# Optimization experiments

Hardware: AMD Instinct MI355X
Metric: run time of the kernel (lower is better)

## Reference

```python
import jax, jax.numpy as jnp
import numpy as np

B, T, IDIM, HDIM, K, LMAX, NLAYERS = 64, 1024, 120, 320, 72, 96, 3
LAMB = 0.1
NEG = -1e30


def lse3(a, b, c):
    m = jnp.maximum(jnp.maximum(a, b), c)
    return m + jnp.log(jnp.exp(a - m) + jnp.exp(b - m) + jnp.exp(c - m))


def _lstm_dir(x, Wih, Whh, bb):
    # x: [B,T,D] -> h: [B,T,H]; PyTorch gate order i,f,g,o
    gx = jnp.einsum('btd,gd->tbg', x, Wih) + bb  # [T,B,4H]
    def step(carry, g):
        h, c = carry
        g = g + h @ Whh.T
        i, f, gg, o = jnp.split(g, 4, axis=-1)
        c = jax.nn.sigmoid(f) * c + jax.nn.sigmoid(i) * jnp.tanh(gg)
        h = jax.nn.sigmoid(o) * jnp.tanh(c)
        return (h, c), h
    h0 = jnp.zeros((x.shape[0], HDIM), x.dtype)
    _, hs = jax.lax.scan(step, (h0, h0), gx)
    return hs.transpose(1, 0, 2)


def _rev(x, lengths):
    # reverse each sequence within its valid length (packed-sequence semantics)
    t = jnp.arange(x.shape[1])
    idx = jnp.where(t[None, :] < lengths[:, None], lengths[:, None] - 1 - t[None, :], t[None, :])
    return jnp.take_along_axis(x, idx[:, :, None], axis=1)


def _blstm_layer(x, Wih_f, Whh_f, b_f, Wih_b, Whh_b, b_b, lengths):
    hf = _lstm_dir(x, Wih_f, Whh_f, b_f)
    hb = _rev(_lstm_dir(_rev(x, lengths), Wih_b, Whh_b, b_b), lengths)
    return jnp.concatenate([hf, hb], axis=2)


def _ctc_forward(logp, labels, in_lens, lab_lens):
    # standard CTC alpha recursion (blank=0), log-space, vectorized over batch
    Bn, Tn, _ = logp.shape
    S = 2 * LMAX + 1
    ext = jnp.zeros((Bn, S), jnp.int32).at[:, 1::2].set(labels)  # blank-interleaved labels
    em = jnp.take_along_axis(logp, jnp.broadcast_to(ext[:, None, :], (Bn, Tn, S)), axis=2)
    em = em.transpose(1, 0, 2)  # [T,B,S]
    s_idx = jnp.arange(S)
    prev_lab = jnp.concatenate([jnp.full((Bn, 2), -1, jnp.int32), ext[:, :-2]], axis=1)
    can_skip = ((s_idx[None, :] % 2) == 1) & (ext != prev_lab)
    valid_s = s_idx[None, :] < (2 * lab_lens[:, None] + 1)
    alpha0 = jnp.full((Bn, S), NEG, logp.dtype)
    alpha0 = alpha0.at[:, 0].set(em[0][:, 0]).at[:, 1].set(em[0][:, 1])
    alpha0 = jnp.where(valid_s, alpha0, NEG)
    def step(alpha, inp):
        em_t, t = inp
        a2 = jnp.concatenate([jnp.full((Bn, 1), NEG, alpha.dtype), alpha[:, :-1]], axis=1)
        a3 = jnp.concatenate([jnp.full((Bn, 2), NEG, alpha.dtype), alpha[:, :-2]], axis=1)
        a3 = jnp.where(can_skip, a3, NEG)
        new = lse3(alpha, a2, a3) + em_t
        new = jnp.where(valid_s, new, NEG)
        new = jnp.where((t < in_lens)[:, None], new, alpha)  # freeze past utterance end
        return new, None
    alpha, _ = jax.lax.scan(step, alpha0, (em[1:], jnp.arange(1, Tn)))
    last = 2 * lab_lens
    aL = jnp.take_along_axis(alpha, last[:, None], axis=1)[:, 0]
    aLm1 = jnp.take_along_axis(alpha, (last - 1)[:, None], axis=1)[:, 0]
    return jnp.logaddexp(aL, aLm1)  # log p(labels | x)


def setup_inputs():
    key = jax.random.key(0)
    ks = jax.random.split(key, 12)
    H4 = 4 * HDIM
    s = 0.05
    return dict(
        logits=jax.random.normal(ks[0], (B, T, IDIM), jnp.float32),
        labels_padded=jax.random.randint(ks[1], (B, LMAX), 1, K).astype(jnp.int32),
        input_lengths=jax.random.randint(ks[2], (B,), T // 2, T + 1).astype(jnp.int32),
        label_lengths=jax.random.randint(ks[3], (B,), LMAX // 2, LMAX + 1).astype(jnp.int32),
        Wih0=jax.random.normal(ks[4], (2, H4, IDIM), jnp.float32) * s,
        Whh0=jax.random.normal(ks[5], (2, H4, HDIM), jnp.float32) * s,
        b0=jnp.zeros((2, H4), jnp.float32),
        Wih=jax.random.normal(ks[6], (NLAYERS - 1, 2, H4, 2 * HDIM), jnp.float32) * s,
        Whh=jax.random.normal(ks[7], (NLAYERS - 1, 2, H4, HDIM), jnp.float32) * s,
        b=jnp.zeros((NLAYERS - 1, 2, H4), jnp.float32),
        W_lin=jax.random.normal(ks[8], (K, 2 * HDIM), jnp.float32) * s,
        b_lin=jnp.zeros((K,), jnp.float32),
    )


def reference(logits, labels_padded, input_lengths, label_lengths, Wih0, Whh0, b0, Wih, Whh, b, W_lin, b_lin):
    # sort by input length descending (mirrors torch.sort + index_select)
    order = jnp.argsort(-input_lengths)
    logits = logits[order]
    labels_padded = labels_padded[order]
    input_lengths = input_lengths[order]
    label_lengths = label_lengths[order]
    # 3-layer BLSTM encoder
    x = _blstm_layer(logits, Wih0[0], Whh0[0], b0[0], Wih0[1], Whh0[1], b0[1], input_lengths)
    for l in range(NLAYERS - 1):
        x = _blstm_layer(x, Wih[l, 0], Whh[l, 0], b[l, 0], Wih[l, 1], Whh[l, 1], b[l, 1], input_lengths)
    netout = jax.nn.log_softmax(x @ W_lin.T + b_lin, axis=2)  # [B,T,K]
    # CTC-CRF: numerator = CTC alpha log-prob; denominator = free-running partition
    num = _ctc_forward(netout, labels_padded, input_lengths, label_lengths)
    tmask = jnp.arange(netout.shape[1])[None, :] < input_lengths[:, None]
    den = jnp.sum(jnp.where(tmask, jax.nn.logsumexp(netout, axis=2), 0.0), axis=1)
    return jnp.mean(den - (1.0 + LAMB) * num)
```

## Files before the change

kernel.cpp:

```cpp
#include <hip/hip_runtime.h>
#include <cstdint>
#include <cstddef>


typedef _Float16 f16;
typedef _Float16 h2v   __attribute__((ext_vector_type(2)));
typedef _Float16 f16x4v __attribute__((ext_vector_type(4)));
typedef _Float16 f16x8 __attribute__((ext_vector_type(8)));
typedef float    f32x4 __attribute__((ext_vector_type(4)));
typedef uint32_t u32x4 __attribute__((ext_vector_type(4)));

#define NEGF (-1e30f)
#define CT 128

__device__ __forceinline__ float dot2f(h2v a, h2v b, float c) {
#if __has_builtin(__builtin_amdgcn_fdot2)
  return __builtin_amdgcn_fdot2(a, b, c, false);
#else
  return c + (float)a.x * (float)b.x + (float)a.y * (float)b.y;
#endif
}

__device__ __forceinline__ float fast_rcp(float x) {
#if __has_builtin(__builtin_amdgcn_rcpf)
  return __builtin_amdgcn_rcpf(x);
#else
  return 1.f / x;
#endif
}
__device__ __forceinline__ float fsigm(float x) { return fast_rcp(1.f + __expf(-x)); }
__device__ __forceinline__ float ftanh(float x) { return 1.f - 2.f * fast_rcp(1.f + __expf(2.f * x)); }

__device__ __forceinline__ float fexp2(float x) {
#if __has_builtin(__builtin_amdgcn_exp2f)
  return __builtin_amdgcn_exp2f(x);
#else
  return exp2f(x);
#endif
}
__device__ __forceinline__ float flog2(float x) {
#if __has_builtin(__builtin_amdgcn_logf)
  return __builtin_amdgcn_logf(x);
#else
  return log2f(x);
#endif
}

__device__ __forceinline__ void bar_lds() {
  __builtin_amdgcn_sched_barrier(0);
  asm volatile("s_waitcnt lgkmcnt(0)" ::: "memory");
  __builtin_amdgcn_s_barrier();
  __builtin_amdgcn_sched_barrier(0);
}

__device__ __forceinline__ void stage16(f16* lds, const f16* g) {
#if __has_builtin(__builtin_amdgcn_global_load_lds)
  __builtin_amdgcn_global_load_lds(
      (const __attribute__((address_space(1))) uint32_t*)g,
      (__attribute__((address_space(3))) uint32_t*)lds, 16, 0, 0);
#else
  int lane = threadIdx.x & 63;
  *(f16x8*)&lds[lane * 8] = *(const f16x8*)g;
#endif
}


__global__ void conv_logits(const float* __restrict__ src, f16* __restrict__ dst) {
  int idx = blockIdx.x * 256 + threadIdx.x;
  int row = idx >> 7, k = idx & 127;
  dst[idx] = (f16)((k < 120) ? src[(size_t)row * 120 + k] : 0.f);
}

__global__ void conv_wt0(const float* __restrict__ w, f16* __restrict__ dst) {
  int idx = blockIdx.x * 256 + threadIdx.x;
  int n = idx >> 7, k = idx & 127;
  dst[idx] = (f16)((k < 120) ? w[(size_t)n * 120 + k] : 0.f);
}

__global__ void conv_copy(const float* __restrict__ src, f16* __restrict__ dst, int count) {
  int idx = blockIdx.x * 256 + threadIdx.x;
  if (idx < count) dst[idx] = (f16)src[idx];
}

__global__ void conv_wtl(const float* __restrict__ w, f16* __restrict__ dst) {
  int idx = blockIdx.x * 256 + threadIdx.x;
  int n = idx / 640, k = idx % 640;
  dst[idx] = (f16)((n < 72) ? w[(size_t)n * 640 + k] : 0.f);
}

__global__ void conv_whh(const float* __restrict__ whh0, const float* __restrict__ whh,
                         uint32_t* __restrict__ dst) {
  int o = blockIdx.x * 256 + threadIdx.x;
  int tid = o & 511;
  int g  = o >> 9;
  int j  = g % 40;
  int g2 = g / 40;
  int i  = g2 % 5;
  int g3 = g2 / 5;
  int hf = g3 & 1, slot = g3 >> 1;
  int tau = i * 512 + tid;
  int lr = tau >> 2, kq = tau & 3;
  int gate = lr / 160, u = lr - gate * 160;
  int r = gate * 320 + hf * 160 + u;
  int k = kq * 80 + j * 2;
  const float* srcm = (slot < 2) ? (whh0 + ((size_t)slot * 1280 + r) * 320)
                                 : (whh  + ((size_t)(slot - 2) * 1280 + r) * 320);
  f16 lo = (f16)srcm[k], hi = (f16)srcm[k + 1];
  dst[o] = (uint32_t)__builtin_bit_cast(unsigned short, lo) |
           ((uint32_t)__builtin_bit_cast(unsigned short, hi) << 16);
}

__global__ __launch_bounds__(256)
void gemm_chunk(const f16* __restrict__ A, const f16* __restrict__ W,
                f16* __restrict__ gxc, const int* __restrict__ lens,
                int lda, int kTiles, int c0) {
  __shared__ __align__(16) f16 As[128 * 32];
  __shared__ __align__(16) f16 Ws[2][128 * 32];
  const int tid = threadIdx.x;
  const int lane = tid & 63, wid = tid >> 6;
  const int wm = wid >> 1, wn = wid & 1;
  const int dir = blockIdx.y >> 6, b = blockIdx.y & 63;
  const int n0 = blockIdx.x * 256;
  const int r_base = lane >> 2;
  const int chs = ((((lane & 3) + (r_base >> 1)) & 3)) * 8;
  const int len = lens[b];

  f32x4 acc[4][8] = {};

  for (int kt = 0; kt < kTiles; ++kt) {
    const int k0 = kt * 32;
    __syncthreads();
#pragma unroll
    for (int hh = 0; hh < 2; ++hh) {
      const int c = wid * 2 + hh;
      const int j = c * 16 + r_base;
      const int s = c0 * CT + j;
      const int tt = dir ? ((s < len) ? (len - 1 - s) : s) : s;
      stage16(&As[c * 512], A + (size_t)(b * 1024 + tt) * lda + k0 + chs);
    }
#pragma unroll
    for (int hh = 0; hh < 4; ++hh) {
      const int c = wid * 4 + hh;
      const int tile = c >> 3, cc = c & 7;
      stage16(&Ws[tile][cc * 512],
              W + (size_t)(dir * 1280 + n0 + tile * 128 + cc * 16 + r_base) * lda + k0 + chs);
    }
    __syncthreads();

    const int q = lane >> 4;
    const int l15 = lane & 15;
    const int cs = (q - (l15 >> 1)) & 3;
    const int rofs = l15 * 32 + cs * 8;
    f16x8 av[4], wv0[4], wv1[4];
#pragma unroll
    for (int i = 0; i < 4; ++i)
      av[i] = *(const f16x8*)&As[(wm * 4 + i) * 512 + rofs];
#pragma unroll
    for (int i = 0; i < 4; ++i) {
      wv0[i] = *(const f16x8*)&Ws[0][(wn * 4 + i) * 512 + rofs];
      wv1[i] = *(const f16x8*)&Ws[1][(wn * 4 + i) * 512 + rofs];
    }
#pragma unroll
    for (int i = 0; i < 4; ++i)
#pragma unroll
      for (int j = 0; j < 4; ++j) {
        acc[i][j]     = __builtin_amdgcn_mfma_f32_16x16x32_f16(av[i], wv0[j], acc[i][j], 0, 0, 0);
        acc[i][4 + j] = __builtin_amdgcn_mfma_f32_16x16x32_f16(av[i], wv1[j], acc[i][4 + j], 0, 0, 0);
      }
  }

  const int r0 = (lane >> 4) * 4, cn = lane & 15;
  const size_t obase = (size_t)(dir * 64 + b) * CT;
#pragma unroll
  for (int i = 0; i < 4; ++i) {
    const int m = wm * 64 + i * 16 + r0;
#pragma unroll
    for (int j = 0; j < 4; ++j) {
      const int n = n0 + wn * 64 + j * 16 + cn;
#pragma unroll
      for (int r = 0; r < 4; ++r) {
        gxc[(obase + m + r) * 1280 + n]       = (f16)acc[i][j][r];
        gxc[(obase + m + r) * 1280 + n + 128] = (f16)acc[i][4 + j][r];
      }
    }
  }
}

__global__ void __launch_bounds__(512)
__attribute__((amdgpu_waves_per_eu(2, 2)))
lstm_scan_chunk(const volatile uint32_t* wbuf,
                const f16* __restrict__ gxc,
                const float* __restrict__ bias,
                const int* __restrict__ lens,
                f16* xnext,
                uint32_t* xq,
                f16* hsave,
                float* csave,
                int layer, int c0) {
  const int wg = blockIdx.x;
  const int half = wg >> 7;
  const int bd = wg & 127;
  const int b = bd >> 1, dir = bd & 1;
  const int tid = threadIdx.x;

  __shared__ __align__(16) f16 hbuf[320];
  __shared__ float ylds[640];
  __shared__ __align__(16) f16 hstage[64 * 160];

  h2v w[5][40];
  {
    const volatile uint32_t* wb =
        wbuf + (size_t)((layer * 2 + dir) * 2 + half) * 200 * 512;
#pragma unroll
    for (int i = 0; i < 5; ++i)
#pragma unroll
      for (int j = 0; j < 40; ++j) {
        uint32_t v = wb[(i * 40 + j) * 512 + tid];
        w[i][j] = __builtin_bit_cast(h2v, v);
      }
  }
  if (tid < 320) hbuf[tid] = (c0 == 0) ? (f16)0.f : hsave[bd * 320 + tid];

  const int len = lens[b];
  const int kq = tid & 3;
  const int qi = tid >> 2;
  const int gu = half * 160 + tid;
  float c_state = 0.f;
  float bi = 0.f, bff = 0.f, bg = 0.f, bo = 0.f;
  if (tid < 160) {
    if (c0 > 0) c_state = csave[wg * 160 + tid];
    const float* bp = bias + dir * 1280 + gu;
    bi = bp[0]; bff = bp[320]; bg = bp[640]; bo = bp[960];
  }
  __syncthreads();

  const size_t grow0 = (size_t)(dir * 64 + b) * CT;

  float gxi = 0.f, gxf = 0.f, gxg = 0.f, gxo = 0.f;
  if (tid < 160) {
    const f16* gp = gxc + grow0 * 1280 + gu;
    gxi = (float)gp[0]; gxf = (float)gp[320]; gxg = (float)gp[640]; gxo = (float)gp[960];
  }

  for (int tl = 0; tl < CT; ++tl) {
    const int s = c0 * CT + tl;
    const uint32_t tag = (uint32_t)(layer * 1024 + s + 1);

    float nxi = 0.f, nxf = 0.f, nxg = 0.f, nxo = 0.f;
    if (tid < 160 && tl + 1 < CT) {
      const f16* gp = gxc + (grow0 + tl + 1) * 1280 + gu;
      nxi = (float)gp[0]; nxf = (float)gp[320]; nxg = (float)gp[640]; nxo = (float)gp[960];
    }

    float a0 = 0.f, a1 = 0.f, a2 = 0.f, a3 = 0.f, a4 = 0.f;
    {
      const u32x4* h4 = (const u32x4*)hbuf;
#pragma unroll
      for (int jb = 0; jb < 5; ++jb) {
        u32x4 p = h4[kq * 10 + jb * 2];
        u32x4 q = h4[kq * 10 + jb * 2 + 1];
        h2v hr[8];
#pragma unroll
        for (int j = 0; j < 4; ++j) hr[j] = __builtin_bit_cast(h2v, p[j]);
#pragma unroll
        for (int j = 0; j < 4; ++j) hr[4 + j] = __builtin_bit_cast(h2v, q[j]);
#pragma unroll
        for (int j = 0; j < 8; ++j) {
          a0 = dot2f(w[0][jb * 8 + j], hr[j], a0);
          a1 = dot2f(w[1][jb * 8 + j], hr[j], a1);
          a2 = dot2f(w[2][jb * 8 + j], hr[j], a2);
          a3 = dot2f(w[3][jb * 8 + j], hr[j], a3);
          a4 = dot2f(w[4][jb * 8 + j], hr[j], a4);
        }
      }
    }
    {
      float av[5] = {a0, a1, a2, a3, a4};
#pragma unroll
      for (int i = 0; i < 5; ++i) {
        float v = av[i];
        v += __shfl_xor(v, 1, 64);
        v += __shfl_xor(v, 2, 64);
        if (kq == 0) ylds[i * 128 + qi] = v;
      }
    }

    if ((tl & 31) == 0 && tl > 0) {
      const int tw = tl - 32;
#pragma unroll
      for (int it = 0; it < 2; ++it) {
        const int slot = it * 512 + tid;
        if (slot < 640) {
          const int r = (int)(((unsigned)slot * 52429u) >> 20);
          const int j = slot - r * 20;
          const int sp = c0 * CT + tw + r;
          const int ttp = dir ? ((sp < len) ? (len - 1 - sp) : sp) : sp;
          f16x8 v = *(const f16x8*)&hstage[((tw + r) & 63) * 160 + j * 8];
          *(f16x8*)&xnext[(size_t)(b * 1024 + ttp) * 640 + dir * 320 + half * 160 + j * 8] = v;
        }
      }
    }
    bar_lds();

    if (tid < 160) {
      const int u = tid;
      float pi = ylds[u]       + gxi + bi;
      float pf = ylds[160 + u] + gxf + bff;
      float pg = ylds[320 + u] + gxg + bg;
      float po = ylds[480 + u] + gxo + bo;
      float ig = fsigm(pi);
      float fg = fsigm(pf);
      float gg = ftanh(pg);
      float og = fsigm(po);
      c_state = fg * c_state + ig * gg;
      float hv = og * ftanh(c_state);
      const f16 hh = (f16)hv;
      const uint32_t word = (tag << 16) |
                            (uint32_t)__builtin_bit_cast(unsigned short, hh);
      __hip_atomic_store(&xq[((bd * 2 + half) * 2 + (s & 1)) * 160 + u], word,
                         __ATOMIC_RELAXED, __HIP_MEMORY_SCOPE_AGENT);
      hbuf[gu] = hh;
      hstage[(tl & 63) * 160 + u] = hh;
    } else if (tid >= 256 && tid < 416) {
      const int u = tid - 256;
      uint32_t pw;
      int spins = 0;
      do {
        pw = __hip_atomic_load(&xq[((bd * 2 + (1 - half)) * 2 + (s & 1)) * 160 + u],
                               __ATOMIC_RELAXED, __HIP_MEMORY_SCOPE_AGENT);
      } while ((pw >> 16) != tag && ++spins < 200000);
      hbuf[(1 - half) * 160 + u] =
          __builtin_bit_cast(f16, (unsigned short)(pw & 0xffffu));
    }
    bar_lds();

    gxi = nxi; gxf = nxf; gxg = nxg; gxo = nxo;
  }

  {
    const int tw = CT - 32;
#pragma unroll
    for (int it = 0; it < 2; ++it) {
      const int slot = it * 512 + tid;
      if (slot < 640) {
        const int r = (int)(((unsigned)slot * 52429u) >> 20);
        const int j = slot - r * 20;
        const int sp = c0 * CT + tw + r;
        const int ttp = dir ? ((sp < len) ? (len - 1 - sp) : sp) : sp;
        f16x8 v = *(const f16x8*)&hstage[((tw + r) & 63) * 160 + j * 8];
        *(f16x8*)&xnext[(size_t)(b * 1024 + ttp) * 640 + dir * 320 + half * 160 + j * 8] = v;
      }
    }
  }
  if (tid < 160) {
    hsave[bd * 320 + gu] = hbuf[gu];
    csave[wg * 160 + tid] = c_state;
  }
}

__global__ __launch_bounds__(256)
void gemm_proj(const f16* __restrict__ A, const f16* __restrict__ W,
               float* __restrict__ outf, int lda, int kTiles, int ldo) {
  __shared__ __align__(16) f16 As[128 * 32];
  __shared__ __align__(16) f16 Ws[128 * 32];
  const int tid = threadIdx.x;
  const int lane = tid & 63, wid = tid >> 6;
  const int wm = wid >> 1, wn = wid & 1;
  const int m0 = blockIdx.y * 128, n0 = blockIdx.x * 128;
  const int r_base = lane >> 2;
  const int chs = ((((lane & 3) + (r_base >> 1)) & 3)) * 8;

  f32x4 acc[4][4] = {};

  for (int kt = 0; kt < kTiles; ++kt) {
    const int k0 = kt * 32;
    __syncthreads();
#pragma unroll
    for (int hh = 0; hh < 2; ++hh) {
      const int c = wid * 2 + hh;
      stage16(&As[c * 512], A + (size_t)(m0 + c * 16 + r_base) * lda + k0 + chs);
      stage16(&Ws[c * 512], W + (size_t)(n0 + c * 16 + r_base) * lda + k0 + chs);
    }
    __syncthreads();

    const int q = lane >> 4;
    const int l15 = lane & 15;
    const int cs = (q - (l15 >> 1)) & 3;
    const int rofs = l15 * 32 + cs * 8;
    f16x8 av[4], wv[4];
#pragma unroll
    for (int i = 0; i < 4; ++i)
      av[i] = *(const f16x8*)&As[(wm * 4 + i) * 512 + rofs];
#pragma unroll
    for (int i = 0; i < 4; ++i)
      wv[i] = *(const f16x8*)&Ws[(wn * 4 + i) * 512 + rofs];
#pragma unroll
    for (int i = 0; i < 4; ++i)
#pragma unroll
      for (int j = 0; j < 4; ++j)
        acc[i][j] = __builtin_amdgcn_mfma_f32_16x16x32_f16(av[i], wv[j], acc[i][j], 0, 0, 0);
  }

  const int r0 = (lane >> 4) * 4, cn = lane & 15;
#pragma unroll
  for (int i = 0; i < 4; ++i) {
    const int m = m0 + wm * 64 + i * 16 + r0;
#pragma unroll
    for (int j = 0; j < 4; ++j) {
      const int n = n0 + wn * 64 + j * 16 + cn;
#pragma unroll
      for (int r = 0; r < 4; ++r)
        outf[(size_t)(m + r) * ldo + n] = acc[i][j][r];
    }
  }
}

__global__ void lse_kernel(const float* __restrict__ Z, const float* __restrict__ b_lin,
                           float* __restrict__ lseout) {
  int row = blockIdx.x * 4 + (threadIdx.x >> 6);
  int l = threadIdx.x & 63;
  const float* z = Z + (size_t)row * 128;
  float v0 = (l < 72) ? z[l] + b_lin[l] : NEGF;
  float v1 = (l < 8) ? z[l + 64] + b_lin[l + 64] : NEGF;
  float m = fmaxf(v0, v1);
#pragma unroll
  for (int o = 32; o; o >>= 1) m = fmaxf(m, __shfl_xor(m, o, 64));
  float s = ((l < 72) ? __expf(v0 - m) : 0.f) + ((l < 8) ? __expf(v1 - m) : 0.f);
#pragma unroll
  for (int o = 32; o; o >>= 1) s += __shfl_xor(s, o, 64);
  if (l == 0) lseout[row] = m + __logf(s);
}

__global__ void emz_kernel(const float* __restrict__ Z, const float* __restrict__ lse,
                           const float* __restrict__ b_lin,
                           const int* __restrict__ labels,
                           f16* __restrict__ emc) {
  const int b = blockIdx.y;
  const int t0 = blockIdx.x * 4;
  const int tid = threadIdx.x;
  __shared__ int ext[200];
  __shared__ float bls[200];
  if (tid < 200) {
    int e = (tid < 193 && (tid & 1)) ? labels[b * 96 + (tid >> 1)] : 0;
    ext[tid] = e;
    bls[tid] = b_lin[e];
  }
  __syncthreads();
#pragma unroll
  for (int dt = 0; dt < 4; ++dt) {
    const int t = t0 + dt;
    const float lst = lse[b * 1024 + t];
    const float* zr = Z + ((size_t)(b * 1024 + t)) * 128;
    for (int s = tid; s < 200; s += 256)
      emc[((size_t)(b * 1024 + t)) * 200 + s] =
          (f16)((zr[ext[s]] + bls[s] - lst) * 1.4426950408889634f);
  }
}

__global__ void ctc_kernel(const f16* __restrict__ emc,
                           const int* __restrict__ labels, const int* __restrict__ inlen,
                           const int* __restrict__ lablen, float* __restrict__ num) {
  const int b = blockIdx.x;
  const int lane = threadIdx.x;
  __shared__ int ext[200];
  __shared__ float afin[200];

  for (int s = lane; s < 200; s += 64)
    ext[s] = (s < 193 && (s & 1)) ? labels[b * 96 + (s >> 1)] : 0;
  __syncthreads();

  const int L = lablen[b], len = inlen[b];
  const int Send = 2 * L + 1;
  const f16* eb = emc + (size_t)b * 1024 * 200;

  float a[4];
  bool  skp[4], val[4];
#pragma unroll
  for (int j = 0; j < 4; ++j) {
    const int s = lane * 4 + j;
    val[j] = (s < Send) && (s < 193);
    skp[j] = (s < 193) && (s & 1) && (s >= 2) && (ext[s] != ext[s - 2]);
  }
  {
    f16x4v e0 = *(const f16x4v*)&eb[lane * 4];
#pragma unroll
    for (int j = 0; j < 4; ++j) {
      const int s = lane * 4 + j;
      a[j] = (s <= 1 && val[j]) ? (float)e0[j] : NEGF;
    }
  }

  auto step = [&](f16x4v ev) {
    float p3 = __shfl_up(a[3], 1, 64);
    float p2 = __shfl_up(a[2], 1, 64);
    if (lane == 0) { p3 = NEGF; p2 = NEGF; }
    const float x2[4] = {p3, a[0], a[1], a[2]};
    const float x3[4] = {p2, p3, a[0], a[1]};
#pragma unroll
    for (int j = 0; j < 4; ++j) {
      const float xa = a[j], xb = x2[j];
      const float xc = skp[j] ? x3[j] : NEGF;
      const float m = fmaxf(xa, fmaxf(xb, xc));
      const float sum = fexp2(xa - m) + fexp2(xb - m) + fexp2(xc - m);
      const float nv = m + flog2(sum) + (float)ev[j];
      a[j] = val[j] ? nv : NEGF;
    }
  };

  f16x4v ring[8];
#pragma unroll
  for (int d = 1; d <= 8; ++d) {
    const int r = (d < len) ? d : (len - 1);
    ring[d & 7] = *(const f16x4v*)&eb[(size_t)r * 200 + lane * 4];
  }

  int t = 1;
  for (; t + 8 <= len; t += 8) {
#pragma unroll
    for (int k = 0; k < 8; ++k) {
      const int slot = (1 + k) & 7;
      f16x4v ev = ring[slot];
      const int tp = t + k + 8;
      if (tp < len)
        ring[slot] = *(const f16x4v*)&eb[(size_t)tp * 200 + lane * 4];
      step(ev);
    }
  }
  for (; t < len; ++t)
    step(*(const f16x4v*)&eb[(size_t)t * 200 + lane * 4]);

#pragma unroll
  for (int j = 0; j < 4; ++j) {
    const int s = lane * 4 + j;
    if (s < 193) afin[s] = a[j];
  }
  __syncthreads();
  if (lane == 0) {
    const float aL = afin[2 * L], aLm1 = afin[2 * L - 1];
    const float m = fmaxf(aL, aLm1);
    num[b] = 0.6931471805599453f * (m + flog2(fexp2(aL - m) + fexp2(aLm1 - m)));
  }
}

__global__ void final_kernel(const float* __restrict__ num, float* __restrict__ out) {
  int l = threadIdx.x;
  float v = -1.1f * num[l];
#pragma unroll
  for (int o = 32; o; o >>= 1) v += __shfl_xor(v, o, 64);
  if (l == 0) out[0] = v * (1.f / 64.f);
}

__global__ void sentinel_kernel(float* __restrict__ out, float code) { out[0] = code; }

extern "C" void kernel_launch(void* const* d_in, const int* in_sizes, int n_in,
                              void* d_out, int out_size, void* d_ws, size_t ws_size,
                              hipStream_t stream) {
  (void)in_sizes; (void)n_in; (void)out_size;

  const float* logits   = (const float*)d_in[0];
  const int*   labels   = (const int*)d_in[1];
  const int*   in_lens  = (const int*)d_in[2];
  const int*   lab_lens = (const int*)d_in[3];
  const float* Wih0     = (const float*)d_in[4];
  const float* Whh0     = (const float*)d_in[5];
  const float* b0       = (const float*)d_in[6];
  const float* Wih      = (const float*)d_in[7];
  const float* Whh      = (const float*)d_in[8];
  const float* bb       = (const float*)d_in[9];
  const float* W_lin    = (const float*)d_in[10];
  const float* b_lin    = (const float*)d_in[11];

  const size_t NEED = (size_t)224 * 1024 * 1024;
  if (ws_size < NEED) {
    sentinel_kernel<<<1, 1, 0, stream>>>((float*)d_out, -(float)(ws_size >> 20));
    return;
  }

  char* ws = (char*)d_ws;
  size_t off = 0;
  auto alloc = [&](size_t bytes) -> char* {
    char* p = ws + off;
    off += (bytes + 255) & ~(size_t)255;
    return p;
  };
  f16*      Xa     = (f16*)alloc((size_t)65536 * 640 * 2);
  f16*      Xb     = (f16*)alloc((size_t)65536 * 640 * 2);
  f16*      gxc    = (f16*)alloc((size_t)2 * 64 * CT * 1280 * 2);
  f16*      Wt0    = (f16*)alloc((size_t)2560 * 128 * 2);
  f16*      Wt12   = (f16*)alloc((size_t)2 * 2560 * 640 * 2);
  f16*      WtL    = (f16*)alloc((size_t)128 * 640 * 2);
  uint32_t* whh16  = (uint32_t*)alloc((size_t)6 * 2 * 200 * 512 * 4);
  float*    lseb   = (float*)alloc((size_t)65536 * 4);
  float*    num    = (float*)alloc(64 * 4);
  uint32_t* xq     = (uint32_t*)alloc((size_t)512 * 160 * 4);
  f16*      hsave  = (f16*)alloc((size_t)128 * 320 * 2);
  float*    csave  = (float*)alloc((size_t)256 * 160 * 4);
  f16*      A0     = Xb;
  float*    Z      = (float*)gxc;
  f16*      emc    = Xa;

  hipMemsetAsync(xq, 0, (size_t)512 * 160 * 4, stream);

  conv_logits<<<32768, 256, 0, stream>>>(logits, A0);
  conv_wt0<<<1280, 256, 0, stream>>>(Wih0, Wt0);
  conv_copy<<<12800, 256, 0, stream>>>(Wih, Wt12, 3276800);
  conv_wtl<<<320, 256, 0, stream>>>(W_lin, WtL);
  conv_whh<<<4800, 256, 0, stream>>>(Whh0, Whh, whh16);

  for (int c = 0; c < 1024 / CT; ++c) {
    gemm_chunk<<<dim3(5, 128), 256, 0, stream>>>(A0, Wt0, gxc, in_lens, 128, 4, c);
    lstm_scan_chunk<<<256, 512, 0, stream>>>(whh16, gxc, b0, in_lens, Xa, xq,
                                             hsave, csave, 0, c);
  }
  for (int c = 0; c < 1024 / CT; ++c) {
    gemm_chunk<<<dim3(5, 128), 256, 0, stream>>>(Xa, Wt12, gxc, in_lens, 640, 20, c);
    lstm_scan_chunk<<<256, 512, 0, stream>>>(whh16, gxc, bb, in_lens, Xb, xq,
                                             hsave, csave, 1, c);
  }
  for (int c = 0; c < 1024 / CT; ++c) {
    gemm_chunk<<<dim3(5, 128), 256, 0, stream>>>(Xb, Wt12 + (size_t)2560 * 640, gxc,
                                                 in_lens, 640, 20, c);
    lstm_scan_chunk<<<256, 512, 0, stream>>>(whh16, gxc, bb + 2560, in_lens, Xa, xq,
                                             hsave, csave, 2, c);
  }
  gemm_proj<<<dim3(1, 512), 256, 0, stream>>>(Xa, WtL, Z, 640, 20, 128);

  lse_kernel<<<16384, 256, 0, stream>>>(Z, b_lin, lseb);
  emz_kernel<<<dim3(256, 64), 256, 0, stream>>>(Z, lseb, b_lin, labels, emc);
  ctc_kernel<<<64, 64, 0, stream>>>(emc, labels, in_lens, lab_lens, num);
  final_kernel<<<1, 64, 0, stream>>>(num, (float*)d_out);
}
```

Baseline: 8.893 ms.

## Quantize recurrent LSTM weights to int8 and run each sequence-direction in one workgroup

Recurrent Whh weights are quantized to int8 with per-row scales, and the hidden state is quantized to int8 (scale 1/127), so the recurrent matvec uses sdot4 instead of fp16 dot2. With weights half the size, the full 1280x320 matrix fits in one 512-thread workgroup's registers. The cross-workgroup atomic spin exchange between two halves is replaced by plain __syncthreads, using 128 workgroups instead of 256. This removes inter-CU synchronization latency on every timestep but quantizes the recurrence, which may lose accuracy through error accumulated over 1024 steps.

After: 9.479 ms. 1.07x slower.

```diff
diff --git a/kernel.cpp b/kernel.cpp
--- a/kernel.cpp
+++ b/kernel.cpp
@@ -13,11 +13,15 @@
 #define NEGF (-1e30f)
 #define CT 128
 
-__device__ __forceinline__ float dot2f(h2v a, h2v b, float c) {
-#if __has_builtin(__builtin_amdgcn_fdot2)
-  return __builtin_amdgcn_fdot2(a, b, c, false);
+__device__ __forceinline__ int dot4i8(int a, int b, int c) {
+#if __has_builtin(__builtin_amdgcn_sdot4)
+  return __builtin_amdgcn_sdot4(a, b, c, false);
 #else
-  return c + (float)a.x * (float)b.x + (float)a.y * (float)b.y;
+  int s = c;
+#pragma unroll
+  for (int e = 0; e < 4; ++e)
+    s += (int)(int8_t)(a >> (8 * e)) * (int)(int8_t)(b >> (8 * e));
+  return s;
 #endif
 }
 
@@ -44,13 +48,6 @@
 #else
   return log2f(x);
 #endif
-}
-
-__device__ __forceinline__ void bar_lds() {
-  __builtin_amdgcn_sched_barrier(0);
-  asm volatile("s_waitcnt lgkmcnt(0)" ::: "memory");
-  __builtin_amdgcn_s_barrier();
-  __builtin_amdgcn_sched_barrier(0);
 }
 
 __device__ __forceinline__ void stage16(f16* lds, const f16* g) {
@@ -88,26 +85,44 @@
   dst[idx] = (f16)((n < 72) ? w[(size_t)n * 640 + k] : 0.f);
 }
 
-__global__ void conv_whh(const float* __restrict__ whh0, const float* __restrict__ whh,
-                         uint32_t* __restrict__ dst) {
+__global__ void conv_scale(const float* __restrict__ whh0, const float* __restrict__ whh,
+                           float* __restrict__ scales) {
+  int row = blockIdx.x * 4 + (threadIdx.x >> 6);
+  int lane = threadIdx.x & 63;
+  int slot = row / 1280, r = row - slot * 1280;
+  const float* src = (slot < 2) ? (whh0 + ((size_t)slot * 1280 + r) * 320)
+                                : (whh  + ((size_t)(slot - 2) * 1280 + r) * 320);
+  float m = 0.f;
+  for (int k = lane; k < 320; k += 64) m = fmaxf(m, fabsf(src[k]));
+#pragma unroll
+  for (int o = 32; o; o >>= 1) m = fmaxf(m, __shfl_xor(m, o, 64));
+  if (lane == 0) scales[row] = fmaxf(m, 1e-20f) * (1.f / 127.f);
+}
+
+__global__ void conv_wq(const float* __restrict__ whh0, const float* __restrict__ whh,
+                        const float* __restrict__ scales, uint32_t* __restrict__ dst) {
   int o = blockIdx.x * 256 + threadIdx.x;
-  int tid = o & 511;
-  int g  = o >> 9;
-  int j  = g % 40;
-  int g2 = g / 40;
-  int i  = g2 % 5;
-  int g3 = g2 / 5;
-  int hf = g3 & 1, slot = g3 >> 1;
-  int tau = i * 512 + tid;
-  int lr = tau >> 2, kq = tau & 3;
-  int gate = lr / 160, u = lr - gate * 160;
-  int r = gate * 320 + hf * 160 + u;
-  int k = kq * 80 + j * 2;
-  const float* srcm = (slot < 2) ? (whh0 + ((size_t)slot * 1280 + r) * 320)
-                                 : (whh  + ((size_t)(slot - 2) * 1280 + r) * 320);
-  f16 lo = (f16)srcm[k], hi = (f16)srcm[k + 1];
-  dst[o] = (uint32_t)__builtin_bit_cast(unsigned short, lo) |
-           ((uint32_t)__builtin_bit_cast(unsigned short, hi) << 16);
+  int t = o & 511;
+  int g = o >> 9;
+  int j = g % 20;
+  int g2 = g / 20;
+  int i = g2 % 10;
+  int slot = g2 / 10;
+  int qi = t >> 2, kq = t & 3;
+  int r = i * 128 + qi;
+  int k0 = kq * 80 + j * 4;
+  const float* src = (slot < 2) ? (whh0 + ((size_t)slot * 1280 + r) * 320)
+                                : (whh  + ((size_t)(slot - 2) * 1280 + r) * 320);
+  float s = scales[slot * 1280 + r];
+  float rs = fast_rcp(s);
+  uint32_t w = 0;
+#pragma unroll
+  for (int e = 0; e < 4; ++e) {
+    float q = rintf(src[k0 + e] * rs);
+    q = fminf(fmaxf(q, -127.f), 127.f);
+    w |= ((uint32_t)(uint8_t)(int8_t)(int)q) << (8 * e);
+  }
+  dst[o] = w;
 }
 
 __global__ __launch_bounds__(256)
@@ -188,97 +203,98 @@
 
 __global__ void __launch_bounds__(512)
 __attribute__((amdgpu_waves_per_eu(2, 2)))
-lstm_scan_chunk(const volatile uint32_t* wbuf,
+lstm_scan_chunk(const volatile uint32_t* wqbuf,
+                const float* __restrict__ scales,
                 const f16* __restrict__ gxc,
                 const float* __restrict__ bias,
                 const int* __restrict__ lens,
                 f16* xnext,
-                uint32_t* xq,
                 f16* hsave,
                 float* csave,
                 int layer, int c0) {
   const int wg = blockIdx.x;
-  const int half = wg >> 7;
-  const int bd = wg & 127;
-  const int b = bd >> 1, dir = bd & 1;
+  const int b = wg >> 1, dir = wg & 1;
   const int tid = threadIdx.x;
-
-  __shared__ __align__(16) f16 hbuf[320];
-  __shared__ float ylds[640];
-  __shared__ __align__(16) f16 hstage[64 * 160];
-
-  h2v w[5][40];
+  const int kq = tid & 3, qi = tid >> 2;
+  const int slot = layer * 2 + dir;
+
+  __shared__ __align__(16) uint32_t hqw[80];
+  __shared__ int ylds[1280];
+  __shared__ __align__(16) f16 hstage[64 * 320];
+
+  uint32_t w[10][20];
   {
-    const volatile uint32_t* wb =
-        wbuf + (size_t)((layer * 2 + dir) * 2 + half) * 200 * 512;
-#pragma unroll
-    for (int i = 0; i < 5; ++i)
-#pragma unroll
-      for (int j = 0; j < 40; ++j) {
-        uint32_t v = wb[(i * 40 + j) * 512 + tid];
-        w[i][j] = __builtin_bit_cast(h2v, v);
-      }
-  }
-  if (tid < 320) hbuf[tid] = (c0 == 0) ? (f16)0.f : hsave[bd * 320 + tid];
+    const volatile uint32_t* wb = wqbuf + (size_t)slot * 10 * 20 * 512;
+#pragma unroll
+    for (int i = 0; i < 10; ++i)
+#pragma unroll
+      for (int j = 0; j < 20; ++j)
+        w[i][j] = wb[(i * 20 + j) * 512 + tid];
+  }
 
   const int len = lens[b];
-  const int kq = tid & 3;
-  const int qi = tid >> 2;
-  const int gu = half * 160 + tid;
-  float c_state = 0.f;
+  float c_state = 0.f, h_cur = 0.f;
   float bi = 0.f, bff = 0.f, bg = 0.f, bo = 0.f;
-  if (tid < 160) {
-    if (c0 > 0) c_state = csave[wg * 160 + tid];
-    const float* bp = bias + dir * 1280 + gu;
+  float ps0 = 0.f, ps1 = 0.f, ps2 = 0.f, ps3 = 0.f;
+  if (tid < 320) {
+    float hv0 = (c0 == 0) ? 0.f : (float)hsave[wg * 320 + tid];
+    h_cur = hv0;
+    ((uint8_t*)hqw)[tid] = (uint8_t)(int8_t)(int)rintf(hv0 * 127.f);
+    if (c0 > 0) c_state = csave[wg * 320 + tid];
+    const float* bp = bias + dir * 1280 + tid;
     bi = bp[0]; bff = bp[320]; bg = bp[640]; bo = bp[960];
+    const float* sp = scales + slot * 1280 + tid;
+    ps0 = sp[0] * (1.f / 127.f);
+    ps1 = sp[320] * (1.f / 127.f);
+    ps2 = sp[640] * (1.f / 127.f);
+    ps3 = sp[960] * (1.f / 127.f);
   }
   __syncthreads();
 
   const size_t grow0 = (size_t)(dir * 64 + b) * CT;
 
   float gxi = 0.f, gxf = 0.f, gxg = 0.f, gxo = 0.f;
-  if (tid < 160) {
-    const f16* gp = gxc + grow0 * 1280 + gu;
+  if (tid < 320) {
+    const f16* gp = gxc + grow0 * 1280 + tid;
     gxi = (float)gp[0]; gxf = (float)gp[320]; gxg = (float)gp[640]; gxo = (float)gp[960];
   }
 
   for (int tl = 0; tl < CT; ++tl) {
-    const int s = c0 * CT + tl;
-    const uint32_t tag = (uint32_t)(layer * 1024 + s + 1);
-
     float nxi = 0.f, nxf = 0.f, nxg = 0.f, nxo = 0.f;
-    if (tid < 160 && tl + 1 < CT) {
-      const f16* gp = gxc + (grow0 + tl + 1) * 1280 + gu;
+    if (tid < 320 && tl + 1 < CT) {
+      const f16* gp = gxc + (grow0 + tl + 1) * 1280 + tid;
       nxi = (float)gp[0]; nxf = (float)gp[320]; nxg = (float)gp[640]; nxo = (float)gp[960];
     }
 
-    float a0 = 0.f, a1 = 0.f, a2 = 0.f, a3 = 0.f, a4 = 0.f;
+    int acc0 = 0, acc1 = 0, acc2 = 0, acc3 = 0, acc4 = 0;
+    int acc5 = 0, acc6 = 0, acc7 = 0, acc8 = 0, acc9 = 0;
     {
-      const u32x4* h4 = (const u32x4*)hbuf;
+      const u32x4* hv4 = (const u32x4*)&hqw[kq * 20];
 #pragma unroll
       for (int jb = 0; jb < 5; ++jb) {
-        u32x4 p = h4[kq * 10 + jb * 2];
-        u32x4 q = h4[kq * 10 + jb * 2 + 1];
-        h2v hr[8];
-#pragma unroll
-        for (int j = 0; j < 4; ++j) hr[j] = __builtin_bit_cast(h2v, p[j]);
-#pragma unroll
-        for (int j = 0; j < 4; ++j) hr[4 + j] = __builtin_bit_cast(h2v, q[j]);
-#pragma unroll
-        for (int j = 0; j < 8; ++j) {
-          a0 = dot2f(w[0][jb * 8 + j], hr[j], a0);
-          a1 = dot2f(w[1][jb * 8 + j], hr[j], a1);
-          a2 = dot2f(w[2][jb * 8 + j], hr[j], a2);
-          a3 = dot2f(w[3][jb * 8 + j], hr[j], a3);
-          a4 = dot2f(w[4][jb * 8 + j], hr[j], a4);
+        u32x4 hv = hv4[jb];
+#pragma unroll
+        for (int e = 0; e < 4; ++e) {
+          const int j = jb * 4 + e;
+          const int hword = (int)hv[e];
+          acc0 = dot4i8((int)w[0][j], hword, acc0);
+          acc1 = dot4i8((int)w[1][j], hword, acc1);
+          acc2 = dot4i8((int)w[2][j], hword, acc2);
+          acc3 = dot4i8((int)w[3][j], hword, acc3);
+          acc4 = dot4i8((int)w[4][j], hword, acc4);
+          acc5 = dot4i8((int)w[5][j], hword, acc5);
+          acc6 = dot4i8((int)w[6][j], hword, acc6);
+          acc7 = dot4i8((int)w[7][j], hword, acc7);
+          acc8 = dot4i8((int)w[8][j], hword, acc8);
+          acc9 = dot4i8((int)w[9][j], hword, acc9);
         }
       }
     }
     {
-      float av[5] = {a0, a1, a2, a3, a4};
-#pragma unroll
-      for (int i = 0; i < 5; ++i) {
-        float v = av[i];
+      int av[10] = {acc0, acc1, acc2, acc3, acc4, acc5, acc6, acc7, acc8, acc9};
+#pragma unroll
+      for (int i = 0; i < 10; ++i) {
+        int v = av[i];
         v += __shfl_xor(v, 1, 64);
         v += __shfl_xor(v, 2, 64);
         if (kq == 0) ylds[i * 128 + qi] = v;
@@ -288,51 +304,37 @@
     if ((tl & 31) == 0 && tl > 0) {
       const int tw = tl - 32;
 #pragma unroll
-      for (int it = 0; it < 2; ++it) {
-        const int slot = it * 512 + tid;
-        if (slot < 640) {
-          const int r = (int)(((unsigned)slot * 52429u) >> 20);
-          const int j = slot - r * 20;
+      for (int it = 0; it < 3; ++it) {
+        const int slt = it * 512 + tid;
+        if (slt < 1280) {
+          const int r = (int)(((unsigned)slt * 1639u) >> 16);
+          const int j = slt - r * 40;
           const int sp = c0 * CT + tw + r;
           const int ttp = dir ? ((sp < len) ? (len - 1 - sp) : sp) : sp;
-          f16x8 v = *(const f16x8*)&hstage[((tw + r) & 63) * 160 + j * 8];
-          *(f16x8*)&xnext[(size_t)(b * 1024 + ttp) * 640 + dir * 320 + half * 160 + j * 8] = v;
+          f16x8 v = *(const f16x8*)&hstage[((tw + r) & 63) * 320 + j * 8];
+          *(f16x8*)&xnext[(size_t)(b * 1024 + ttp) * 640 + dir * 320 + j * 8] = v;
         }
       }
     }
-    bar_lds();
-
-    if (tid < 160) {
+    __syncthreads();
+
+    if (tid < 320) {
       const int u = tid;
-      float pi = ylds[u]       + gxi + bi;
-      float pf = ylds[160 + u] + gxf + bff;
-      float pg = ylds[320 + u] + gxg + bg;
-      float po = ylds[480 + u] + gxo + bo;
+      float pi = ps0 * (float)ylds[u]       + gxi + bi;
+      float pf = ps1 * (float)ylds[u + 320] + gxf + bff;
+      float pg = ps2 * (float)ylds[u + 640] + gxg + bg;
+      float po = ps3 * (float)ylds[u + 960] + gxo + bo;
       float ig = fsigm(pi);
       float fg = fsigm(pf);
       float gg = ftanh(pg);
       float og = fsigm(po);
       c_state = fg * c_state + ig * gg;
       float hv = og * ftanh(c_state);
-      const f16 hh = (f16)hv;
-      const uint32_t word = (tag << 16) |
-                            (uint32_t)__builtin_bit_cast(unsigned short, hh);
-      __hip_atomic_store(&xq[((bd * 2 + half) * 2 + (s & 1)) * 160 + u], word,
-                         __ATOMIC_RELAXED, __HIP_MEMORY_SCOPE_AGENT);
-      hbuf[gu] = hh;
-      hstage[(tl & 63) * 160 + u] = hh;
-    } else if (tid >= 256 && tid < 416) {
-      const int u = tid - 256;
-      uint32_t pw;
-      int spins = 0;
-      do {
-        pw = __hip_atomic_load(&xq[((bd * 2 + (1 - half)) * 2 + (s & 1)) * 160 + u],
-                               __ATOMIC_RELAXED, __HIP_MEMORY_SCOPE_AGENT);
-      } while ((pw >> 16) != tag && ++spins < 200000);
-      hbuf[(1 - half) * 160 + u] =
-          __builtin_bit_cast(f16, (unsigned short)(pw & 0xffffu));
-    }
-    bar_lds();
+      h_cur = hv;
+      hstage[(tl & 63) * 320 + u] = (f16)hv;
+      ((uint8_t*)hqw)[u] = (uint8_t)(int8_t)(int)rintf(hv * 127.f);
+    }
+    __syncthreads();
 
     gxi = nxi; gxf = nxf; gxg = nxg; gxo = nxo;
   }
@@ -340,21 +342,21 @@
   {
     const int tw = CT - 32;
 #pragma unroll
-    for (int it = 0; it < 2; ++it) {
-      const int slot = it * 512 + tid;
-      if (slot < 640) {
-        const int r = (int)(((unsigned)slot * 52429u) >> 20);
-        const int j = slot - r * 20;
+    for (int it = 0; it < 3; ++it) {
+      const int slt = it * 512 + tid;
+      if (slt < 1280) {
+        const int r = (int)(((unsigned)slt * 1639u) >> 16);
+        const int j = slt - r * 40;
         const int sp = c0 * CT + tw + r;
         const int ttp = dir ? ((sp < len) ? (len - 1 - sp) : sp) : sp;
-        f16x8 v = *(const f16x8*)&hstage[((tw + r) & 63) * 160 + j * 8];
-        *(f16x8*)&xnext[(size_t)(b * 1024 + ttp) * 640 + dir * 320 + half * 160 + j * 8] = v;
+        f16x8 v = *(const f16x8*)&hstage[((tw + r) & 63) * 320 + j * 8];
+        *(f16x8*)&xnext[(size_t)(b * 1024 + ttp) * 640 + dir * 320 + j * 8] = v;
       }
     }
   }
-  if (tid < 160) {
-    hsave[bd * 320 + gu] = hbuf[gu];
-    csave[wg * 160 + tid] = c_state;
+  if (tid < 320) {
+    hsave[wg * 320 + tid] = (f16)h_cur;
+    csave[wg * 320 + tid] = c_state;
   }
 }
 
@@ -589,38 +591,37 @@
   f16*      Wt0    = (f16*)alloc((size_t)2560 * 128 * 2);
   f16*      Wt12   = (f16*)alloc((size_t)2 * 2560 * 640 * 2);
   f16*      WtL    = (f16*)alloc((size_t)128 * 640 * 2);
-  uint32_t* whh16  = (uint32_t*)alloc((size_t)6 * 2 * 200 * 512 * 4);
+  uint32_t* wqi    = (uint32_t*)alloc((size_t)6 * 10 * 20 * 512 * 4);
+  float*    scales = (float*)alloc((size_t)6 * 1280 * 4);
   float*    lseb   = (float*)alloc((size_t)65536 * 4);
   float*    num    = (float*)alloc(64 * 4);
-  uint32_t* xq     = (uint32_t*)alloc((size_t)512 * 160 * 4);
   f16*      hsave  = (f16*)alloc((size_t)128 * 320 * 2);
-  float*    csave  = (float*)alloc((size_t)256 * 160 * 4);
+  float*    csave  = (float*)alloc((size_t)128 * 320 * 4);
   f16*      A0     = Xb;
   float*    Z      = (float*)gxc;
   f16*      emc    = Xa;
-
-  hipMemsetAsync(xq, 0, (size_t)512 * 160 * 4, stream);
 
   conv_logits<<<32768, 256, 0, stream>>>(logits, A0);
   conv_wt0<<<1280, 256, 0, stream>>>(Wih0, Wt0);
   conv_copy<<<12800, 256, 0, stream>>>(Wih, Wt12, 3276800);
   conv_wtl<<<320, 256, 0, stream>>>(W_lin, WtL);
-  conv_whh<<<4800, 256, 0, stream>>>(Whh0, Whh, whh16);
+  conv_scale<<<1920, 256, 0, stream>>>(Whh0, Whh, scales);
+  conv_wq<<<2400, 256, 0, stream>>>(Whh0, Whh, scales, wqi);
 
   for (int c = 0; c < 1024 / CT; ++c) {
     gemm_chunk<<<dim3(5, 128), 256, 0, stream>>>(A0, Wt0, gxc, in_lens, 128, 4, c);
-    lstm_scan_chunk<<<256, 512, 0, stream>>>(whh16, gxc, b0, in_lens, Xa, xq,
+    lstm_scan_chunk<<<128, 512, 0, stream>>>(wqi, scales, gxc, b0, in_lens, Xa,
                                              hsave, csave, 0, c);
   }
   for (int c = 0; c < 1024 / CT; ++c) {
     gemm_chunk<<<dim3(5, 128), 256, 0, stream>>>(Xa, Wt12, gxc, in_lens, 640, 20, c);
-    lstm_scan_chunk<<<256, 512, 0, stream>>>(whh16, gxc, bb, in_lens, Xb, xq,
+    lstm_scan_chunk<<<128, 512, 0, stream>>>(wqi, scales, gxc, bb, in_lens, Xb,
                                              hsave, csave, 1, c);
   }
   for (int c = 0; c < 1024 / CT; ++c) {
     gemm_chunk<<<dim3(5, 128), 256, 0, stream>>>(Xb, Wt12 + (size_t)2560 * 640, gxc,
                                                  in_lens, 640, 20, c);
-    lstm_scan_chunk<<<256, 512, 0, stream>>>(whh16, gxc, bb + 2560, in_lens, Xa, xq,
+    lstm_scan_chunk<<<128, 512, 0, stream>>>(wqi, scales, gxc, bb + 2560, in_lens, Xa,
                                              hsave, csave, 2, c);
   }
   gemm_proj<<<dim3(1, 512), 256, 0, stream>>>(Xa, WtL, Z, 640, 20, 128);
```
